# Optimization experiments

Measured on AMD Instinct MI355X. Metric: run time of the kernel, lower is better.

The kernel has to match this reference:

```python
import jax, jax.numpy as jnp
import numpy as np

WINDOW = (2, 6, 12)  # (Wz, Wy, Wx)
HEADS = 6


def _position_index(window):
    Wz, Wy, Wx = window
    cz, cy, cx = np.arange(Wz), np.arange(Wy), np.arange(Wx)
    coords = np.stack(np.meshgrid(cz, cy, cx, indexing='ij'))  # [3, Wz, Wy, Wx]
    cf = coords.reshape(3, -1)                                  # [3, N]
    rel = cf[:, :, None] - cf[:, None, :]                       # [3, N, N]
    rel = rel.transpose(1, 2, 0).astype(np.int64)               # [N, N, 3]
    rel[:, :, 0] += Wz - 1
    rel[:, :, 1] += Wy - 1
    rel[:, :, 2] += Wx - 1
    rel[:, :, 0] *= 2 * Wy - 1
    return jnp.asarray(rel.sum(-1).reshape(-1))                 # [N*N]


def setup_inputs() -> dict:
    key = jax.random.key(0)
    ks = jax.random.split(key, 7)
    dim, N, B_, nW = 192, 144, 1024, 512
    table_rows = (2 * WINDOW[2] - 1) * (2 * WINDOW[1] - 1) * (2 * WINDOW[0] - 1)  # 759
    return {
        'x': jax.random.normal(ks[0], (B_, N, dim), jnp.float32),
        'mask': jax.random.normal(ks[1], (nW, N, N), jnp.float32),
        'w_qkv': jax.random.normal(ks[2], (dim, 3 * dim), jnp.float32) * 0.02,
        'b_qkv': jax.random.normal(ks[3], (3 * dim,), jnp.float32) * 0.02,
        'w_o': jax.random.normal(ks[4], (dim, dim), jnp.float32) * 0.02,
        'b_o': jax.random.normal(ks[5], (dim,), jnp.float32) * 0.02,
        'bias_table': jax.random.normal(ks[6], (table_rows, 1, HEADS), jnp.float32) * 0.02,
    }


def reference(x, mask, w_qkv, b_qkv, w_o, b_o, bias_table):
    B_, N, dim = x.shape
    H = HEADS
    hd = dim // H
    scale = hd ** -0.5

    qkv = x @ w_qkv + b_qkv                              # [B_, N, 3*dim]
    qkv = qkv.reshape(B_, N, 3, H, hd).transpose(2, 0, 3, 1, 4)
    q, k, v = qkv[0], qkv[1], qkv[2]                     # [B_, H, N, hd]

    attn = jnp.einsum('bhnd,bhmd->bhnm', q * scale, k)   # [B_, H, N, N]

    pos_idx = _position_index(WINDOW)                    # [N*N] int constant
    bias = bias_table[pos_idx].reshape(N, N, H).transpose(2, 0, 1)  # [H, N, N]
    attn = attn + bias[None]

    nW = mask.shape[0]
    attn = attn.reshape(B_ // nW, nW, H, N, N) + mask[None, :, None]
    attn = jax.nn.softmax(attn.reshape(B_, H, N, N), axis=-1)

    out = jnp.einsum('bhnm,bhmd->bhnd', attn, v)         # [B_, H, N, hd]
    out = out.transpose(0, 2, 1, 3).reshape(B_, N, dim)
    return out @ w_o + b_o
```

## Files before the change

### kernel.cpp

```cpp
#include <hip/hip_runtime.h>

typedef __attribute__((ext_vector_type(4))) float  f32x4;
typedef __attribute__((ext_vector_type(4))) float  float4v;
typedef __attribute__((ext_vector_type(4))) short  short4v;
typedef __attribute__((ext_vector_type(8))) short  short8v;
typedef __attribute__((ext_vector_type(8))) __bf16 bf16x8;

union Frag { short4v h[2]; short8v s8; };

__device__ __forceinline__ short f2bf(float f) {
  unsigned u = __builtin_bit_cast(unsigned, f);
  u = (u + 0x7fffu + ((u >> 16) & 1u)) >> 16;
  return (short)u;
}

__device__ __forceinline__ f32x4 mfma_bf16(const Frag& a, const Frag& b, f32x4 c) {
  return __builtin_amdgcn_mfma_f32_16x16x32_bf16(
      __builtin_bit_cast(bf16x8, a.s8), __builtin_bit_cast(bf16x8, b.s8), c, 0, 0, 0);
}

__device__ __forceinline__ int poscode(int i) {
  int z = (i >= 72) ? 1 : 0;
  int rem = i - 72 * z;
  int y = rem / 12;
  return 11 * z + y + (rem - 12 * y);
}

__global__ __launch_bounds__(256) void k_transpose_w(
    const float* __restrict__ w_qkv, const float* __restrict__ w_o,
    short* __restrict__ wtq, short* __restrict__ wto) {
  int idx = blockIdx.x * 256 + threadIdx.x;
  if (idx < 110592) {
    int k = idx / 576, c = idx % 576;
    wtq[c * 192 + k] = f2bf(w_qkv[idx]);
  } else {
    int j = idx - 110592;
    int k = j / 192, c = j % 192;
    wto[c * 192 + k] = f2bf(w_o[j]);
  }
}

__global__ __launch_bounds__(256, 2) void k_qkv(
    const float* __restrict__ x, const float* __restrict__ bqkv,
    const short* __restrict__ wtq, short* __restrict__ qkv) {
  __shared__ short a_lds[64][200];
  __shared__ short bT[576][40];
  const int tid = threadIdx.x;
  const int lane = tid & 63, wv = tid >> 6;
  const int l15 = lane & 15, lg = lane >> 4;
  const int row0 = blockIdx.x * 64;

#pragma unroll
  for (int i = 0; i < 12; ++i) {
    int flat = tid + 256 * i;
    int r = flat / 48, c4 = flat % 48;
    float4v xv = *(const float4v*)&x[(size_t)(row0 + r) * 192 + c4 * 4];
    short4v sv = { f2bf(xv[0]), f2bf(xv[1]), f2bf(xv[2]), f2bf(xv[3]) };
    *(short4v*)&a_lds[r][c4 * 4] = sv;
  }

  f32x4 acc[36];
#pragma unroll
  for (int i = 0; i < 36; ++i) acc[i] = f32x4{0.f, 0.f, 0.f, 0.f};

  for (int kc = 0; kc < 6; ++kc) {
    __syncthreads();
#pragma unroll
    for (int i = 0; i < 18; ++i) {
      int flat = tid + 256 * i;
      int c = flat >> 3, kk = (flat & 7) << 2;
      *(short4v*)&bT[c][kk] = *(const short4v*)&wtq[c * 192 + kc * 32 + kk];
    }
    __syncthreads();
    Frag a;
    a.h[0] = *(const short4v*)&a_lds[wv * 16 + l15][kc * 32 + lg * 4];
    a.h[1] = *(const short4v*)&a_lds[wv * 16 + l15][kc * 32 + lg * 4 + 16];
#pragma unroll
    for (int cf = 0; cf < 36; ++cf) {
      Frag bw;
      bw.h[0] = *(const short4v*)&bT[cf * 16 + l15][lg * 4];
      bw.h[1] = *(const short4v*)&bT[cf * 16 + l15][lg * 4 + 16];
      acc[cf] = mfma_bf16(a, bw, acc[cf]);
    }
  }

#pragma unroll
  for (int cf = 0; cf < 36; ++cf) {
    int c = cf * 16 + l15;
    int part = c / 192, rem = c % 192;
    int h = rem >> 5, d = rem & 31;
    float bias = bqkv[c];
    float scale = (part == 0) ? 0.17677669529663687f : 1.0f;
#pragma unroll
    for (int r = 0; r < 4; ++r) {
      int g = row0 + wv * 16 + lg * 4 + r;
      int b_ = g / 144, n = g - b_ * 144;
      float v = (acc[cf][r] + bias) * scale;
      qkv[(size_t)((part * 1024 + b_) * 6 + h) * 4608 + n * 32 + d] = f2bf(v);
    }
  }
}

__global__ __launch_bounds__(512, 2) void k_attn(
    const short* __restrict__ qkv, const float* __restrict__ mask,
    const float* __restrict__ btab, float* __restrict__ out) {
  __shared__ short k_l[6][144][40];
  __shared__ short vt[6][32][152];
  const int tid = threadIdx.x;
  const int lane = tid & 63, wv = tid >> 6;
  const int l15 = lane & 15, lg = lane >> 4;

  const int bid = blockIdx.x;
  const int b = ((bid >> 4) << 3) + (bid & 7) + (((bid >> 3) & 1) << 9);
  const int wm = b & 511;

  const size_t kbase = (size_t)(1024 + b) * 6 * 4608;
#pragma unroll
  for (int i = 0; i < 7; ++i) {
    int flat = tid + 512 * i;
    if (flat < 3456) {
      int h = flat / 576, r = flat % 576;
      int n = r >> 2, d8 = (r & 3) * 8;
      *(short8v*)&k_l[h][n][d8] =
          *(const short8v*)&qkv[kbase + (size_t)h * 4608 + n * 32 + d8];
    }
  }
  const size_t vbase = (size_t)(2048 + b) * 6 * 4608;
#pragma unroll
  for (int i = 0; i < 14; ++i) {
    int flat = tid + 512 * i;
    if (flat < 6912) {
      int h = flat / 1152, r = flat % 1152;
      int n = r >> 3, d4 = (r & 7) * 4;
      short4v vv = *(const short4v*)&qkv[vbase + (size_t)h * 4608 + n * 32 + d4];
      vt[h][d4 + 0][n] = vv[0];
      vt[h][d4 + 1][n] = vv[1];
      vt[h][d4 + 2][n] = vv[2];
      vt[h][d4 + 3][n] = vv[3];
    }
  }
  __syncthreads();

  int cnb6[9];
#pragma unroll
  for (int cf = 0; cf < 9; ++cf) cnb6[cf] = 6 * poscode(cf * 16 + lg * 4);
  const float* maskw = &mask[(size_t)wm * 20736];
  const size_t qb = (size_t)b * 6 * 4608;

  f32x4 mrow[9];
  int C0 = 0, q = 0;
  for (int unit = 0; unit < 7; ++unit) {
    int t, h;
    if (unit < 6) { t = wv; h = unit; }
    else { if (wv >= 6) break; t = 8; h = wv; }
    if (unit == 0 || unit == 6) {
      q = t * 16 + l15;
#pragma unroll
      for (int cf = 0; cf < 9; ++cf)
        mrow[cf] = *(const float4v*)&maskw[q * 144 + cf * 16 + lg * 4];
      C0 = (poscode(q) + 27) * 6;
    }

    const short* qrow = &qkv[qb + (size_t)h * 4608 + q * 32];
    Frag aq;
    aq.h[0] = *(const short4v*)&qrow[lg * 4];
    aq.h[1] = *(const short4v*)&qrow[lg * 4 + 16];

    f32x4 s[9];
#pragma unroll
    for (int cf = 0; cf < 9; ++cf) {
      Frag bk;
      bk.h[0] = *(const short4v*)&k_l[h][cf * 16 + l15][lg * 4];
      bk.h[1] = *(const short4v*)&k_l[h][cf * 16 + l15][lg * 4 + 16];
      s[cf] = mfma_bf16(bk, aq, f32x4{0.f, 0.f, 0.f, 0.f});
    }
#pragma unroll
    for (int cf = 0; cf < 9; ++cf) {
      const int i0 = C0 + h - cnb6[cf];
#pragma unroll
      for (int reg = 0; reg < 4; ++reg)
        s[cf][reg] += mrow[cf][reg] + btab[i0 - 6 * reg];
    }

    float mx = s[0][0];
#pragma unroll
    for (int cf = 0; cf < 9; ++cf)
#pragma unroll
      for (int reg = 0; reg < 4; ++reg) mx = fmaxf(mx, s[cf][reg]);
    mx = fmaxf(mx, __shfl_xor(mx, 16, 64));
    mx = fmaxf(mx, __shfl_xor(mx, 32, 64));
    float sum = 0.f;
#pragma unroll
    for (int cf = 0; cf < 9; ++cf)
#pragma unroll
      for (int reg = 0; reg < 4; ++reg) {
        float e = __expf(s[cf][reg] - mx);
        s[cf][reg] = e;
        sum += e;
      }
    sum += __shfl_xor(sum, 16, 64);
    sum += __shfl_xor(sum, 32, 64);
    const float rinv = 1.0f / sum;
#pragma unroll
    for (int cf = 0; cf < 9; ++cf)
#pragma unroll
      for (int reg = 0; reg < 4; ++reg) s[cf][reg] *= rinv;

    f32x4 o0 = {0.f, 0.f, 0.f, 0.f}, o1 = {0.f, 0.f, 0.f, 0.f};
#pragma unroll
    for (int kc = 0; kc < 5; ++kc) {
      Frag ap, b0, b1;
      ap.h[0] = short4v{ f2bf(s[2 * kc][0]), f2bf(s[2 * kc][1]),
                         f2bf(s[2 * kc][2]), f2bf(s[2 * kc][3]) };
      b0.h[0] = *(const short4v*)&vt[h][l15][kc * 32 + lg * 4];
      b1.h[0] = *(const short4v*)&vt[h][16 + l15][kc * 32 + lg * 4];
      if (kc < 4) {
        ap.h[1] = short4v{ f2bf(s[2 * kc + 1][0]), f2bf(s[2 * kc + 1][1]),
                           f2bf(s[2 * kc + 1][2]), f2bf(s[2 * kc + 1][3]) };
        b0.h[1] = *(const short4v*)&vt[h][l15][kc * 32 + lg * 4 + 16];
        b1.h[1] = *(const short4v*)&vt[h][16 + l15][kc * 32 + lg * 4 + 16];
      } else {
        ap.h[1] = short4v{0, 0, 0, 0};
        b0.h[1] = short4v{0, 0, 0, 0};
        b1.h[1] = short4v{0, 0, 0, 0};
      }
      o0 = mfma_bf16(ap, b0, o0);
      o1 = mfma_bf16(ap, b1, o1);
    }
#pragma unroll
    for (int rr = 0; rr < 4; ++rr) {
      const int m = t * 16 + lg * 4 + rr;
      const size_t base = (size_t)(b * 144 + m) * 192 + h * 32;
      out[base + l15]      = o0[rr];
      out[base + 16 + l15] = o1[rr];
    }
  }
}

__global__ __launch_bounds__(256, 2) void k_oproj(
    float* __restrict__ io, const float* __restrict__ bo,
    const short* __restrict__ wto) {
  __shared__ short a_lds[64][200];
  __shared__ short bT[192][40];
  const int tid = threadIdx.x;
  const int lane = tid & 63, wv = tid >> 6;
  const int l15 = lane & 15, lg = lane >> 4;
  const int row0 = blockIdx.x * 64;

#pragma unroll
  for (int i = 0; i < 12; ++i) {
    int flat = tid + 256 * i;
    int r = flat / 48, c4 = flat % 48;
    float4v xv = *(const float4v*)&io[(size_t)(row0 + r) * 192 + c4 * 4];
    short4v sv = { f2bf(xv[0]), f2bf(xv[1]), f2bf(xv[2]), f2bf(xv[3]) };
    *(short4v*)&a_lds[r][c4 * 4] = sv;
  }

  f32x4 acc[12];
#pragma unroll
  for (int i = 0; i < 12; ++i) acc[i] = f32x4{0.f, 0.f, 0.f, 0.f};

  for (int kc = 0; kc < 6; ++kc) {
    __syncthreads();
#pragma unroll
    for (int i = 0; i < 6; ++i) {
      int flat = tid + 256 * i;
      int c = flat >> 3, kk = (flat & 7) << 2;
      *(short4v*)&bT[c][kk] = *(const short4v*)&wto[c * 192 + kc * 32 + kk];
    }
    __syncthreads();
    Frag a;
    a.h[0] = *(const short4v*)&a_lds[wv * 16 + l15][kc * 32 + lg * 4];
    a.h[1] = *(const short4v*)&a_lds[wv * 16 + l15][kc * 32 + lg * 4 + 16];
#pragma unroll
    for (int cf = 0; cf < 12; ++cf) {
      Frag bw;
      bw.h[0] = *(const short4v*)&bT[cf * 16 + l15][lg * 4];
      bw.h[1] = *(const short4v*)&bT[cf * 16 + l15][lg * 4 + 16];
      acc[cf] = mfma_bf16(a, bw, acc[cf]);
    }
  }

#pragma unroll
  for (int cf = 0; cf < 12; ++cf) {
    int c = cf * 16 + l15;
    float bias = bo[c];
#pragma unroll
    for (int r = 0; r < 4; ++r) {
      int g = row0 + wv * 16 + lg * 4 + r;
      io[(size_t)g * 192 + c] = acc[cf][r] + bias;
    }
  }
}

extern "C" void kernel_launch(void* const* d_in, const int* in_sizes, int n_in,
                              void* d_out, int out_size, void* d_ws, size_t ws_size,
                              hipStream_t stream) {
  const float* x    = (const float*)d_in[0];
  const float* mask = (const float*)d_in[1];
  const float* wqkv = (const float*)d_in[2];
  const float* bqkv = (const float*)d_in[3];
  const float* wo   = (const float*)d_in[4];
  const float* bo   = (const float*)d_in[5];
  const float* btab = (const float*)d_in[6];
  float* out = (float*)d_out;

  short* wtq = (short*)d_ws;
  short* wto = wtq + 110592;
  short* qkv = wto + 36864;

  k_transpose_w<<<576, 256, 0, stream>>>(wqkv, wo, wtq, wto);
  k_qkv<<<2304, 256, 0, stream>>>(x, bqkv, wtq, qkv);
  k_attn<<<1024, 512, 0, stream>>>(qkv, mask, btab, out);
  k_oproj<<<2304, 256, 0, stream>>>(out, bo, wto);
}
```

Baseline: 320.5 us.

## Split QKV and attention kernels finer, permute K layout, precompute bias table

The QKV GEMM now splits each row tile into two column halves and reads weight fragments straight from global memory instead of staging them in LDS, which removes the per-chunk barriers. The K dimension is permuted so each lane loads one 8-wide vector per fragment. Attention blocks now handle two heads per window rather than six, with a remapped block order for locality. A new kernel materializes the expanded relative-position bias for all heads so attention reads it with vector loads instead of gathering from the table. The trade-offs are more blocks, reloading the x tile and mask across blocks, and extra global traffic for the bias buffer.

New measurement: 616.2 us. 1.92x slower.

```diff
diff --git a/kernel.cpp b/kernel.cpp
--- a/kernel.cpp
+++ b/kernel.cpp
@@ -24,6 +24,10 @@
   int rem = i - 72 * z;
   int y = rem / 12;
   return 11 * z + y + (rem - 12 * y);
+}
+
+__device__ __forceinline__ int kperm(int r) {
+  return (r & 16) ? (((r - 16) >> 2) * 8 + 4 + (r & 3)) : ((r >> 2) * 8 + (r & 3));
 }
 
 __global__ __launch_bounds__(256) void k_transpose_w(
@@ -32,7 +36,8 @@
   int idx = blockIdx.x * 256 + threadIdx.x;
   if (idx < 110592) {
     int k = idx / 576, c = idx % 576;
-    wtq[c * 192 + k] = f2bf(w_qkv[idx]);
+    int kp = (k & ~31) + kperm(k & 31);
+    wtq[c * 192 + kp] = f2bf(w_qkv[idx]);
   } else {
     int j = idx - 110592;
     int k = j / 192, c = j % 192;
@@ -40,15 +45,26 @@
   }
 }
 
-__global__ __launch_bounds__(256, 2) void k_qkv(
+__global__ __launch_bounds__(256) void k_bias(
+    const float* __restrict__ btab, float* __restrict__ bias6) {
+  int idx = blockIdx.x * 256 + threadIdx.x;
+  if (idx >= 124416) return;
+  int h = idx / 20736, r = idx % 20736, m = r / 144, n = r % 144;
+  bias6[idx] = btab[(poscode(m) - poscode(n) + 27) * 6 + h];
+}
+
+__global__ __launch_bounds__(256, 3) void k_qkv(
     const float* __restrict__ x, const float* __restrict__ bqkv,
     const short* __restrict__ wtq, short* __restrict__ qkv) {
   __shared__ short a_lds[64][200];
-  __shared__ short bT[576][40];
   const int tid = threadIdx.x;
   const int lane = tid & 63, wv = tid >> 6;
   const int l15 = lane & 15, lg = lane >> 4;
-  const int row0 = blockIdx.x * 64;
+
+  const int did = blockIdx.x;
+  const int vid = (did & 7) * 576 + (did >> 3);
+  const int row0 = (vid >> 1) * 64;
+  const int col0 = (vid & 1) * 288;
 
 #pragma unroll
   for (int i = 0; i < 12; ++i) {
@@ -56,39 +72,33 @@
     int r = flat / 48, c4 = flat % 48;
     float4v xv = *(const float4v*)&x[(size_t)(row0 + r) * 192 + c4 * 4];
     short4v sv = { f2bf(xv[0]), f2bf(xv[1]), f2bf(xv[2]), f2bf(xv[3]) };
-    *(short4v*)&a_lds[r][c4 * 4] = sv;
-  }
-
-  f32x4 acc[36];
-#pragma unroll
-  for (int i = 0; i < 36; ++i) acc[i] = f32x4{0.f, 0.f, 0.f, 0.f};
+    int k = c4 * 4, rr = k & 31;
+    int pos = (k & ~31) + ((rr & 16) ? (((rr - 16) >> 2) * 8 + 4) : ((rr >> 2) * 8));
+    *(short4v*)&a_lds[r][pos] = sv;
+  }
+  __syncthreads();
+
+  f32x4 acc[18];
+#pragma unroll
+  for (int i = 0; i < 18; ++i) acc[i] = f32x4{0.f, 0.f, 0.f, 0.f};
 
   for (int kc = 0; kc < 6; ++kc) {
-    __syncthreads();
-#pragma unroll
-    for (int i = 0; i < 18; ++i) {
-      int flat = tid + 256 * i;
-      int c = flat >> 3, kk = (flat & 7) << 2;
-      *(short4v*)&bT[c][kk] = *(const short4v*)&wtq[c * 192 + kc * 32 + kk];
-    }
-    __syncthreads();
     Frag a;
-    a.h[0] = *(const short4v*)&a_lds[wv * 16 + l15][kc * 32 + lg * 4];
-    a.h[1] = *(const short4v*)&a_lds[wv * 16 + l15][kc * 32 + lg * 4 + 16];
-#pragma unroll
-    for (int cf = 0; cf < 36; ++cf) {
+    a.s8 = *(const short8v*)&a_lds[wv * 16 + l15][kc * 32 + lg * 8];
+#pragma unroll
+    for (int cf = 0; cf < 18; ++cf) {
       Frag bw;
-      bw.h[0] = *(const short4v*)&bT[cf * 16 + l15][lg * 4];
-      bw.h[1] = *(const short4v*)&bT[cf * 16 + l15][lg * 4 + 16];
+      bw.s8 = *(const short8v*)&wtq[(col0 + cf * 16 + l15) * 192 + kc * 32 + lg * 8];
       acc[cf] = mfma_bf16(a, bw, acc[cf]);
     }
   }
 
 #pragma unroll
-  for (int cf = 0; cf < 36; ++cf) {
-    int c = cf * 16 + l15;
+  for (int cf = 0; cf < 18; ++cf) {
+    int c = col0 + cf * 16 + l15;
     int part = c / 192, rem = c % 192;
     int h = rem >> 5, d = rem & 31;
+    int dd = (part == 2) ? d : kperm(d);
     float bias = bqkv[c];
     float scale = (part == 0) ? 0.17677669529663687f : 1.0f;
 #pragma unroll
@@ -96,143 +106,133 @@
       int g = row0 + wv * 16 + lg * 4 + r;
       int b_ = g / 144, n = g - b_ * 144;
       float v = (acc[cf][r] + bias) * scale;
-      qkv[(size_t)((part * 1024 + b_) * 6 + h) * 4608 + n * 32 + d] = f2bf(v);
-    }
-  }
-}
-
-__global__ __launch_bounds__(512, 2) void k_attn(
+      qkv[(size_t)((part * 1024 + b_) * 6 + h) * 4608 + n * 32 + dd] = f2bf(v);
+    }
+  }
+}
+
+__global__ __launch_bounds__(256, 3) void k_attn(
     const short* __restrict__ qkv, const float* __restrict__ mask,
-    const float* __restrict__ btab, float* __restrict__ out) {
-  __shared__ short k_l[6][144][40];
-  __shared__ short vt[6][32][152];
+    const float* __restrict__ bias6, float* __restrict__ out) {
+  __shared__ short k_l[2][144][40];
+  __shared__ short vt[2][32][168];
   const int tid = threadIdx.x;
   const int lane = tid & 63, wv = tid >> 6;
   const int l15 = lane & 15, lg = lane >> 4;
 
-  const int bid = blockIdx.x;
-  const int b = ((bid >> 4) << 3) + (bid & 7) + (((bid >> 3) & 1) << 9);
-  const int wm = b & 511;
-
-  const size_t kbase = (size_t)(1024 + b) * 6 * 4608;
-#pragma unroll
-  for (int i = 0; i < 7; ++i) {
-    int flat = tid + 512 * i;
-    if (flat < 3456) {
-      int h = flat / 576, r = flat % 576;
-      int n = r >> 2, d8 = (r & 3) * 8;
-      *(short8v*)&k_l[h][n][d8] =
-          *(const short8v*)&qkv[kbase + (size_t)h * 4608 + n * 32 + d8];
-    }
-  }
-  const size_t vbase = (size_t)(2048 + b) * 6 * 4608;
-#pragma unroll
-  for (int i = 0; i < 14; ++i) {
-    int flat = tid + 512 * i;
-    if (flat < 6912) {
-      int h = flat / 1152, r = flat % 1152;
-      int n = r >> 3, d4 = (r & 7) * 4;
-      short4v vv = *(const short4v*)&qkv[vbase + (size_t)h * 4608 + n * 32 + d4];
-      vt[h][d4 + 0][n] = vv[0];
-      vt[h][d4 + 1][n] = vv[1];
-      vt[h][d4 + 2][n] = vv[2];
-      vt[h][d4 + 3][n] = vv[3];
-    }
+  const int did = blockIdx.x;
+  const int vid = (did & 7) * 384 + (did >> 3);
+  const int wm = vid / 6, r6 = vid - wm * 6;
+  const int b = wm + (r6 >= 3 ? 512 : 0);
+  const int hg = (r6 >= 3) ? r6 - 3 : r6;
+
+  const size_t kbase = (size_t)((1024 + b) * 6 + hg * 2) * 4608;
+#pragma unroll
+  for (int i = 0; i < 5; ++i) {
+    int flat = tid + 256 * i;
+    if (flat < 1152) {
+      int hh = flat / 576, r = flat % 576;
+      int n = r >> 2, j8 = (r & 3) * 8;
+      *(short8v*)&k_l[hh][n][j8] =
+          *(const short8v*)&qkv[kbase + (size_t)hh * 4608 + n * 32 + j8];
+    }
+  }
+#pragma unroll
+  for (int i = 0; i < 4; ++i) {
+    int flat = tid + 256 * i;
+    int hh = flat >> 9, r = flat & 511;
+    int d = r >> 4, jj = r & 15;
+    vt[hh][d][128 + (jj >> 2) * 8 + 4 + (jj & 3)] = 0;
+  }
+  const size_t vbase = (size_t)((2048 + b) * 6 + hg * 2) * 4608;
+#pragma unroll
+  for (int i = 0; i < 9; ++i) {
+    int flat = tid + 256 * i;
+    int hh = flat / 1152, r = flat % 1152;
+    int n = r >> 3, d4 = (r & 7) * 4;
+    short4v vv = *(const short4v*)&qkv[vbase + (size_t)hh * 4608 + n * 32 + d4];
+    int np = (n & ~31) + kperm(n & 31);
+    vt[hh][d4 + 0][np] = vv[0];
+    vt[hh][d4 + 1][np] = vv[1];
+    vt[hh][d4 + 2][np] = vv[2];
+    vt[hh][d4 + 3][np] = vv[3];
   }
   __syncthreads();
 
-  int cnb6[9];
-#pragma unroll
-  for (int cf = 0; cf < 9; ++cf) cnb6[cf] = 6 * poscode(cf * 16 + lg * 4);
   const float* maskw = &mask[(size_t)wm * 20736];
-  const size_t qb = (size_t)b * 6 * 4608;
-
-  f32x4 mrow[9];
-  int C0 = 0, q = 0;
-  for (int unit = 0; unit < 7; ++unit) {
-    int t, h;
-    if (unit < 6) { t = wv; h = unit; }
-    else { if (wv >= 6) break; t = 8; h = wv; }
-    if (unit == 0 || unit == 6) {
-      q = t * 16 + l15;
+  const size_t qb = (size_t)(b * 6 + hg * 2) * 4608;
+
+  for (int tt = wv; tt < 9; tt += 4) {
+    const int q = tt * 16 + l15;
+    f32x4 mrow[9];
+#pragma unroll
+    for (int cf = 0; cf < 9; ++cf)
+      mrow[cf] = *(const float4v*)&maskw[q * 144 + cf * 16 + lg * 4];
+
+    for (int hh = 0; hh < 2; ++hh) {
+      Frag aq;
+      aq.s8 = *(const short8v*)&qkv[qb + (size_t)hh * 4608 + q * 32 + lg * 8];
+
+      f32x4 s[9];
+#pragma unroll
+      for (int cf = 0; cf < 9; ++cf) {
+        Frag bk;
+        bk.s8 = *(const short8v*)&k_l[hh][cf * 16 + l15][lg * 8];
+        s[cf] = mfma_bf16(bk, aq, f32x4{0.f, 0.f, 0.f, 0.f});
+      }
+      const float* brow = &bias6[(size_t)((hg * 2 + hh) * 144 + q) * 144];
+#pragma unroll
+      for (int cf = 0; cf < 9; ++cf) {
+        float4v bv = *(const float4v*)&brow[cf * 16 + lg * 4];
+        s[cf] += mrow[cf] + bv;
+      }
+
+      float mx = s[0][0];
 #pragma unroll
       for (int cf = 0; cf < 9; ++cf)
-        mrow[cf] = *(const float4v*)&maskw[q * 144 + cf * 16 + lg * 4];
-      C0 = (poscode(q) + 27) * 6;
-    }
-
-    const short* qrow = &qkv[qb + (size_t)h * 4608 + q * 32];
-    Frag aq;
-    aq.h[0] = *(const short4v*)&qrow[lg * 4];
-    aq.h[1] = *(const short4v*)&qrow[lg * 4 + 16];
-
-    f32x4 s[9];
-#pragma unroll
-    for (int cf = 0; cf < 9; ++cf) {
-      Frag bk;
-      bk.h[0] = *(const short4v*)&k_l[h][cf * 16 + l15][lg * 4];
-      bk.h[1] = *(const short4v*)&k_l[h][cf * 16 + l15][lg * 4 + 16];
-      s[cf] = mfma_bf16(bk, aq, f32x4{0.f, 0.f, 0.f, 0.f});
-    }
-#pragma unroll
-    for (int cf = 0; cf < 9; ++cf) {
-      const int i0 = C0 + h - cnb6[cf];
-#pragma unroll
-      for (int reg = 0; reg < 4; ++reg)
-        s[cf][reg] += mrow[cf][reg] + btab[i0 - 6 * reg];
-    }
-
-    float mx = s[0][0];
-#pragma unroll
-    for (int cf = 0; cf < 9; ++cf)
-#pragma unroll
-      for (int reg = 0; reg < 4; ++reg) mx = fmaxf(mx, s[cf][reg]);
-    mx = fmaxf(mx, __shfl_xor(mx, 16, 64));
-    mx = fmaxf(mx, __shfl_xor(mx, 32, 64));
-    float sum = 0.f;
-#pragma unroll
-    for (int cf = 0; cf < 9; ++cf)
-#pragma unroll
-      for (int reg = 0; reg < 4; ++reg) {
-        float e = __expf(s[cf][reg] - mx);
-        s[cf][reg] = e;
-        sum += e;
+#pragma unroll
+        for (int reg = 0; reg < 4; ++reg) mx = fmaxf(mx, s[cf][reg]);
+      mx = fmaxf(mx, __shfl_xor(mx, 16, 64));
+      mx = fmaxf(mx, __shfl_xor(mx, 32, 64));
+      float sum = 0.f;
+#pragma unroll
+      for (int cf = 0; cf < 9; ++cf)
+#pragma unroll
+        for (int reg = 0; reg < 4; ++reg) {
+          float e = __expf(s[cf][reg] - mx);
+          s[cf][reg] = e;
+          sum += e;
+        }
+      sum += __shfl_xor(sum, 16, 64);
+      sum += __shfl_xor(sum, 32, 64);
+      const float rinv = 1.0f / sum;
+#pragma unroll
+      for (int cf = 0; cf < 9; ++cf)
+#pragma unroll
+        for (int reg = 0; reg < 4; ++reg) s[cf][reg] *= rinv;
+
+      f32x4 o0 = {0.f, 0.f, 0.f, 0.f}, o1 = {0.f, 0.f, 0.f, 0.f};
+#pragma unroll
+      for (int kc = 0; kc < 5; ++kc) {
+        Frag ap, b0, b1;
+        ap.h[0] = short4v{ f2bf(s[2 * kc][0]), f2bf(s[2 * kc][1]),
+                           f2bf(s[2 * kc][2]), f2bf(s[2 * kc][3]) };
+        ap.h[1] = (kc < 4)
+            ? short4v{ f2bf(s[2 * kc + 1][0]), f2bf(s[2 * kc + 1][1]),
+                       f2bf(s[2 * kc + 1][2]), f2bf(s[2 * kc + 1][3]) }
+            : short4v{0, 0, 0, 0};
+        b0.s8 = *(const short8v*)&vt[hh][l15][kc * 32 + lg * 8];
+        b1.s8 = *(const short8v*)&vt[hh][16 + l15][kc * 32 + lg * 8];
+        o0 = mfma_bf16(ap, b0, o0);
+        o1 = mfma_bf16(ap, b1, o1);
       }
-    sum += __shfl_xor(sum, 16, 64);
-    sum += __shfl_xor(sum, 32, 64);
-    const float rinv = 1.0f / sum;
-#pragma unroll
-    for (int cf = 0; cf < 9; ++cf)
-#pragma unroll
-      for (int reg = 0; reg < 4; ++reg) s[cf][reg] *= rinv;
-
-    f32x4 o0 = {0.f, 0.f, 0.f, 0.f}, o1 = {0.f, 0.f, 0.f, 0.f};
-#pragma unroll
-    for (int kc = 0; kc < 5; ++kc) {
-      Frag ap, b0, b1;
-      ap.h[0] = short4v{ f2bf(s[2 * kc][0]), f2bf(s[2 * kc][1]),
-                         f2bf(s[2 * kc][2]), f2bf(s[2 * kc][3]) };
-      b0.h[0] = *(const short4v*)&vt[h][l15][kc * 32 + lg * 4];
-      b1.h[0] = *(const short4v*)&vt[h][16 + l15][kc * 32 + lg * 4];
-      if (kc < 4) {
-        ap.h[1] = short4v{ f2bf(s[2 * kc + 1][0]), f2bf(s[2 * kc + 1][1]),
-                           f2bf(s[2 * kc + 1][2]), f2bf(s[2 * kc + 1][3]) };
-        b0.h[1] = *(const short4v*)&vt[h][l15][kc * 32 + lg * 4 + 16];
-        b1.h[1] = *(const short4v*)&vt[h][16 + l15][kc * 32 + lg * 4 + 16];
-      } else {
-        ap.h[1] = short4v{0, 0, 0, 0};
-        b0.h[1] = short4v{0, 0, 0, 0};
-        b1.h[1] = short4v{0, 0, 0, 0};
+#pragma unroll
+      for (int rr = 0; rr < 4; ++rr) {
+        const int m = tt * 16 + lg * 4 + rr;
+        const size_t base = (size_t)(b * 144 + m) * 192 + (hg * 2 + hh) * 32;
+        out[base + l15]      = o0[rr];
+        out[base + 16 + l15] = o1[rr];
       }
-      o0 = mfma_bf16(ap, b0, o0);
-      o1 = mfma_bf16(ap, b1, o1);
-    }
-#pragma unroll
-    for (int rr = 0; rr < 4; ++rr) {
-      const int m = t * 16 + lg * 4 + rr;
-      const size_t base = (size_t)(b * 144 + m) * 192 + h * 32;
-      out[base + l15]      = o0[rr];
-      out[base + 16 + l15] = o1[rr];
     }
   }
 }
@@ -305,12 +305,14 @@
   const float* btab = (const float*)d_in[6];
   float* out = (float*)d_out;
 
-  short* wtq = (short*)d_ws;
-  short* wto = wtq + 110592;
-  short* qkv = wto + 36864;
+  short* wtq   = (short*)d_ws;
+  short* wto   = wtq + 110592;
+  short* qkv   = wto + 36864;
+  float* bias6 = (float*)(qkv + 84934656);
 
   k_transpose_w<<<576, 256, 0, stream>>>(wqkv, wo, wtq, wto);
-  k_qkv<<<2304, 256, 0, stream>>>(x, bqkv, wtq, qkv);
-  k_attn<<<1024, 512, 0, stream>>>(qkv, mask, btab, out);
+  k_bias<<<486, 256, 0, stream>>>(btab, bias6);
+  k_qkv<<<4608, 256, 0, stream>>>(x, bqkv, wtq, qkv);
+  k_attn<<<3072, 256, 0, stream>>>(qkv, mask, bias6, out);
   k_oproj<<<2304, 256, 0, stream>>>(out, bo, wto);
 }
```
